# Kernel optimization log

Hardware: AMD Instinct MI355X
Metric: run time of the kernel (lower is better)

## Reference

```python
import jax, jax.numpy as jnp
import numpy as np

NEG_SLOPE = 0.2


def setup_inputs() -> dict:
    key = jax.random.key(0)
    k1, k2, k3 = jax.random.split(key, 3)
    B, C, F_in, F_out = 8, 2048, 64, 64
    node_features = jax.random.normal(k1, (B, C, F_in), dtype=jnp.float32)
    # nn.Linear weight: [out_features, in_features]
    W = jax.random.normal(k2, (F_out, F_in), dtype=jnp.float32) * (1.0 / np.sqrt(F_in))
    # attention vector a: [2*F_out, 1], xavier-uniform style init
    bound = float(np.sqrt(6.0 / (2 * F_out + 1)))
    a = jax.random.uniform(k3, (2 * F_out, 1), dtype=jnp.float32, minval=-bound, maxval=bound)
    return {"node_features": node_features, "W": W, "a": a}


def reference(node_features, W, a):
    # Wh: [B, C, F_out]
    Wh = jnp.einsum("bcf,of->bco", node_features, W)
    F_out = W.shape[0]
    a1 = a[:F_out, 0]  # scores for the i (row) side
    a2 = a[F_out:, 0]  # scores for the j (col) side
    # Decompose concat([Wh_i, Wh_j]) @ a == Wh_i@a1 + Wh_j@a2 (avoids [B,C,C,2F] tensor)
    s1 = Wh @ a1  # [B, C]
    s2 = Wh @ a2  # [B, C]
    e = jax.nn.leaky_relu(s1[:, :, None] + s2[:, None, :], negative_slope=NEG_SLOPE)  # [B,C,C]
    attention = jax.nn.softmax(e, axis=-1)
    out = jnp.einsum("bij,bjo->bio", attention, Wh)  # weighted aggregate
    return jax.nn.elu(out), attention
```

## Files before the change

kernel.cpp:

```cpp
#include <hip/hip_runtime.h>

typedef float f32x4 __attribute__((ext_vector_type(4)));
typedef _Float16 half8 __attribute__((ext_vector_type(8)));

#define NEG 0.2f

__global__ __launch_bounds__(256) void gat_wh_kernel(
    const float* __restrict__ nf, const float* __restrict__ W,
    const float* __restrict__ a, _Float16* __restrict__ whT,
    float* __restrict__ s1g, float* __restrict__ s2g, float* __restrict__ smax)
{
    const int b    = blockIdx.x >> 5;
    const int rb   = blockIdx.x & 31;
    const int row0 = rb * 64;
    const int t    = threadIdx.x;
    const int lane = t & 63;
    const int wv   = t >> 6;

    __shared__ _Float16 whL[64][72];
    __shared__ float    wred[4];

    f32x4 Wreg[16];
    const float* wp = W + lane * 64;
#pragma unroll
    for (int i = 0; i < 16; ++i) Wreg[i] = *(const f32x4*)(wp + i * 4);
    const float a1v = a[lane];
    const float a2v = a[64 + lane];

    const float* nfb = nf + ((long)b * 2048 + row0) * 64;
    float wmax = -3.0e38f;

    for (int g = 0; g < 16; ++g) {
        const int row = g * 4 + wv;
        const f32x4* nfp = (const f32x4*)(nfb + row * 64);
        f32x4 acc = {0.f, 0.f, 0.f, 0.f};
#pragma unroll
        for (int i = 0; i < 16; ++i) acc += nfp[i] * Wreg[i];
        const float wh = acc.x + acc.y + acc.z + acc.w;
        whL[row][lane] = (_Float16)wh;
        float p1 = wh * a1v;
        float p2 = wh * a2v;
#pragma unroll
        for (int m = 32; m >= 1; m >>= 1) {
            p1 += __shfl_xor(p1, m);
            p2 += __shfl_xor(p2, m);
        }
        if (lane == 0) {
            s1g[b * 2048 + row0 + row] = p1;
            s2g[b * 2048 + row0 + row] = p2;
            wmax = fmaxf(wmax, p2);
        }
    }
    if (lane == 0) wred[wv] = wmax;
    __syncthreads();
    if (t == 0)
        smax[blockIdx.x] = fmaxf(fmaxf(wred[0], wred[1]), fmaxf(wred[2], wred[3]));

    const int o = t >> 2;
    const int part = t & 3;
    unsigned int tmp[8];
#pragma unroll
    for (int kk = 0; kk < 8; ++kk) {
        const int j = part * 16 + kk * 2;
        unsigned int lo = *(const unsigned short*)&whL[j][o];
        unsigned int hi = *(const unsigned short*)&whL[j + 1][o];
        tmp[kk] = lo | (hi << 16);
    }
    uint4 v0, v1;
    v0.x = tmp[0]; v0.y = tmp[1]; v0.z = tmp[2]; v0.w = tmp[3];
    v1.x = tmp[4]; v1.y = tmp[5]; v1.z = tmp[6]; v1.w = tmp[7];
    _Float16* dst = whT + ((long)(b * 64 + o) * 2048 + row0 + part * 16);
    *(uint4*)dst = v0;
    *(uint4*)(dst + 8) = v1;
}

__global__ __launch_bounds__(256) void gat_attn_kernel(
    const _Float16* __restrict__ whT, const float* __restrict__ s1g,
    const float* __restrict__ s2g, const float* __restrict__ smax,
    float* __restrict__ outp)
{
    const int b    = blockIdx.x >> 6;
    const int rb   = blockIdx.x & 63;
    const int i0   = rb * 32;
    const int t    = threadIdx.x;
    const int lane = t & 63;
    const int wv   = t >> 6;

    __shared__ __attribute__((aligned(16))) float s2sh[2048];
    __shared__ float s1sh[32], Msh[32], iDsh[32];
    __shared__ float m2sh;
    __shared__ __attribute__((aligned(16))) _Float16 Pl[32][72];
    __shared__ __attribute__((aligned(16))) _Float16 WhL[64][72];

#pragma unroll
    for (int k = 0; k < 8; ++k) s2sh[t + k * 256] = s2g[b * 2048 + t + k * 256];
    if (t < 32) {
        s1sh[t] = s1g[b * 2048 + i0 + t];
        float v = smax[b * 32 + t];
#pragma unroll
        for (int m = 16; m >= 1; m >>= 1) v = fmaxf(v, __shfl_xor(v, m));
        if (t == 0) m2sh = v;
    }
    __syncthreads();

    {
        const float m2  = m2sh;
        const int   r   = t >> 3, q = t & 7;
        const float s1r = s1sh[r];
        const float xm  = s1r + m2;
        const float M   = fmaxf(xm, NEG * xm);
        float acc = 0.f;
        for (int j = q; j < 2048; j += 8) {
            float x = s1r + s2sh[j];
            float e = fmaxf(x, NEG * x);
            acc += __expf(e - M);
        }
        acc += __shfl_xor(acc, 1);
        acc += __shfl_xor(acc, 2);
        acc += __shfl_xor(acc, 4);
        if (q == 0) { Msh[r] = M; iDsh[r] = 1.0f / acc; }
    }
    __syncthreads();

    f32x4 acc0 = {0.f, 0.f, 0.f, 0.f}, acc1 = {0.f, 0.f, 0.f, 0.f};
    const int h  = wv & 1;
    const int cb = (wv >> 1) * 32;
    float* attnb = outp + 1048576 + ((long)b * 2048 + i0) * 2048;
    const _Float16* whTb = whT + (long)b * 64 * 2048;
    const int so = t >> 2, sp = t & 3;

    for (int c = 0; c < 32; ++c) {
        const int j0 = c * 64;
        {
            const uint4* src = (const uint4*)(whTb + (long)so * 2048 + j0 + sp * 16);
            uint4 w0 = src[0], w1 = src[1];
            *(uint4*)&WhL[so][sp * 16]     = w0;
            *(uint4*)&WhL[so][sp * 16 + 8] = w1;
        }
        const float sv = s2sh[j0 + lane];
#pragma unroll
        for (int k = 0; k < 8; ++k) {
            const int r = wv + k * 4;
            float x = s1sh[r] + sv;
            float e = fmaxf(x, NEG * x);
            float p = __expf(e - Msh[r]) * iDsh[r];
            attnb[(long)r * 2048 + j0 + lane] = p;
            Pl[r][lane] = (_Float16)p;
        }
        __syncthreads();
        {
            const int arow  = h * 16 + (lane & 15);
            const int koff  = (lane >> 4) * 8;
            const int brow0 = cb + (lane & 15);
#pragma unroll
            for (int kc = 0; kc < 2; ++kc) {
                half8 av  = *(const half8*)&Pl[arow][kc * 32 + koff];
                half8 bv0 = *(const half8*)&WhL[brow0][kc * 32 + koff];
                half8 bv1 = *(const half8*)&WhL[brow0 + 16][kc * 32 + koff];
                acc0 = __builtin_amdgcn_mfma_f32_16x16x32_f16(av, bv0, acc0, 0, 0, 0);
                acc1 = __builtin_amdgcn_mfma_f32_16x16x32_f16(av, bv1, acc1, 0, 0, 0);
            }
        }
        __syncthreads();
    }

    {
        const int col = lane & 15;
        const int rg  = lane >> 4;
        float* ob = outp + ((long)b * 2048 + i0 + h * 16 + rg * 4) * 64 + cb + col;
#pragma unroll
        for (int r = 0; r < 4; ++r) {
            float x = acc0[r];
            ob[r * 64] = (x > 0.f) ? x : (__expf(x) - 1.0f);
            float y = acc1[r];
            ob[r * 64 + 16] = (y > 0.f) ? y : (__expf(y) - 1.0f);
        }
    }
}

extern "C" void kernel_launch(void* const* d_in, const int* in_sizes, int n_in,
                              void* d_out, int out_size, void* d_ws, size_t ws_size,
                              hipStream_t stream)
{
    (void)in_sizes; (void)n_in; (void)out_size; (void)ws_size;
    const float* nf = (const float*)d_in[0];
    const float* W  = (const float*)d_in[1];
    const float* a  = (const float*)d_in[2];
    float* outp = (float*)d_out;

    char* ws = (char*)d_ws;
    _Float16* whT = (_Float16*)ws;
    float* s1g  = (float*)(ws + 2097152);
    float* s2g  = (float*)(ws + 2097152 + 65536);
    float* smax = (float*)(ws + 2097152 + 131072);

    gat_wh_kernel<<<256, 256, 0, stream>>>(nf, W, a, whT, s1g, s2g, smax);
    gat_attn_kernel<<<512, 256, 0, stream>>>(whT, s1g, s2g, smax, outp);
}
```

Before: 68.91 us.

## Compute attention probabilities directly in MFMA register layout, drop LDS staging and barriers

Result: slower. 86.60 us (+25.7%).

```diff
diff --git a/kernel.cpp b/kernel.cpp
--- a/kernel.cpp
+++ b/kernel.cpp
@@ -89,8 +89,6 @@
     __shared__ __attribute__((aligned(16))) float s2sh[2048];
     __shared__ float s1sh[32], Msh[32], iDsh[32];
     __shared__ float m2sh;
-    __shared__ __attribute__((aligned(16))) _Float16 Pl[32][72];
-    __shared__ __attribute__((aligned(16))) _Float16 WhL[64][72];
 
 #pragma unroll
     for (int k = 0; k < 8; ++k) s2sh[t + k * 256] = s2g[b * 2048 + t + k * 256];
@@ -122,58 +120,70 @@
     }
     __syncthreads();
 
+    const int h    = wv & 1;
+    const int cq   = wv >> 1;
+    const int mloc = h * 16 + (lane & 15);
+    const int g    = lane >> 4;
+    const float s1r = s1sh[mloc];
+    const float Mr  = Msh[mloc];
+    const float iDr = iDsh[mloc];
+
     f32x4 acc0 = {0.f, 0.f, 0.f, 0.f}, acc1 = {0.f, 0.f, 0.f, 0.f};
-    const int h  = wv & 1;
-    const int cb = (wv >> 1) * 32;
-    float* attnb = outp + 1048576 + ((long)b * 2048 + i0) * 2048;
-    const _Float16* whTb = whT + (long)b * 64 * 2048;
-    const int so = t >> 2, sp = t & 3;
+    const _Float16* Bb0 = whT + (long)b * 64 * 2048 + (long)(cq * 32 + (lane & 15)) * 2048 + g * 8;
+    const _Float16* Bb1 = Bb0 + 16 * 2048;
+    float* attnr = outp + 1048576 + ((long)b * 2048 + i0 + mloc) * 2048 + cq * 32 + g * 8;
+    const float* s2p = &s2sh[g * 8];
 
     for (int c = 0; c < 32; ++c) {
         const int j0 = c * 64;
-        {
-            const uint4* src = (const uint4*)(whTb + (long)so * 2048 + j0 + sp * 16);
-            uint4 w0 = src[0], w1 = src[1];
-            *(uint4*)&WhL[so][sp * 16]     = w0;
-            *(uint4*)&WhL[so][sp * 16 + 8] = w1;
-        }
-        const float sv = s2sh[j0 + lane];
-#pragma unroll
-        for (int k = 0; k < 8; ++k) {
-            const int r = wv + k * 4;
-            float x = s1sh[r] + sv;
-            float e = fmaxf(x, NEG * x);
-            float p = __expf(e - Msh[r]) * iDsh[r];
-            attnb[(long)r * 2048 + j0 + lane] = p;
-            Pl[r][lane] = (_Float16)p;
-        }
-        __syncthreads();
-        {
-            const int arow  = h * 16 + (lane & 15);
-            const int koff  = (lane >> 4) * 8;
-            const int brow0 = cb + (lane & 15);
-#pragma unroll
-            for (int kc = 0; kc < 2; ++kc) {
-                half8 av  = *(const half8*)&Pl[arow][kc * 32 + koff];
-                half8 bv0 = *(const half8*)&WhL[brow0][kc * 32 + koff];
-                half8 bv1 = *(const half8*)&WhL[brow0 + 16][kc * 32 + koff];
-                acc0 = __builtin_amdgcn_mfma_f32_16x16x32_f16(av, bv0, acc0, 0, 0, 0);
-                acc1 = __builtin_amdgcn_mfma_f32_16x16x32_f16(av, bv1, acc1, 0, 0, 0);
-            }
-        }
-        __syncthreads();
+        half8 b00 = *(const half8*)(Bb0 + j0);
+        half8 b01 = *(const half8*)(Bb1 + j0);
+        half8 b10 = *(const half8*)(Bb0 + j0 + 32);
+        half8 b11 = *(const half8*)(Bb1 + j0 + 32);
+
+        f32x4 sa0 = *(const f32x4*)(s2p + j0);
+        f32x4 sa1 = *(const f32x4*)(s2p + j0 + 4);
+        f32x4 sb0 = *(const f32x4*)(s2p + j0 + 32);
+        f32x4 sb1 = *(const f32x4*)(s2p + j0 + 36);
+        f32x4 p00, p01, p10, p11;
+        half8 a0, a1;
+#pragma unroll
+        for (int e = 0; e < 4; ++e) {
+            float x, lr, p;
+            x = s1r + sa0[e]; lr = fmaxf(x, NEG * x);
+            p = __expf(lr - Mr) * iDr; p00[e] = p; a0[e] = (_Float16)p;
+            x = s1r + sa1[e]; lr = fmaxf(x, NEG * x);
+            p = __expf(lr - Mr) * iDr; p01[e] = p; a0[e + 4] = (_Float16)p;
+            x = s1r + sb0[e]; lr = fmaxf(x, NEG * x);
+            p = __expf(lr - Mr) * iDr; p10[e] = p; a1[e] = (_Float16)p;
+            x = s1r + sb1[e]; lr = fmaxf(x, NEG * x);
+            p = __expf(lr - Mr) * iDr; p11[e] = p; a1[e + 4] = (_Float16)p;
+        }
+
+        if (cq == 0) {
+            __builtin_nontemporal_store(p00, (f32x4*)(attnr + j0));
+            __builtin_nontemporal_store(p01, (f32x4*)(attnr + j0 + 4));
+        } else {
+            __builtin_nontemporal_store(p10, (f32x4*)(attnr + j0));
+            __builtin_nontemporal_store(p11, (f32x4*)(attnr + j0 + 4));
+        }
+
+        acc0 = __builtin_amdgcn_mfma_f32_16x16x32_f16(a0, b00, acc0, 0, 0, 0);
+        acc1 = __builtin_amdgcn_mfma_f32_16x16x32_f16(a0, b01, acc1, 0, 0, 0);
+        acc0 = __builtin_amdgcn_mfma_f32_16x16x32_f16(a1, b10, acc0, 0, 0, 0);
+        acc1 = __builtin_amdgcn_mfma_f32_16x16x32_f16(a1, b11, acc1, 0, 0, 0);
     }
 
     {
-        const int col = lane & 15;
+        const int col = cq * 32 + (lane & 15);
         const int rg  = lane >> 4;
-        float* ob = outp + ((long)b * 2048 + i0 + h * 16 + rg * 4) * 64 + cb + col;
+        float* ob = outp + ((long)b * 2048 + i0 + h * 16 + rg * 4) * 64 + col;
 #pragma unroll
         for (int r = 0; r < 4; ++r) {
             float x = acc0[r];
-            ob[r * 64] = (x > 0.f) ? x : (__expf(x) - 1.0f);
+            ob[(long)r * 64] = (x > 0.f) ? x : (__expf(x) - 1.0f);
             float y = acc1[r];
-            ob[r * 64 + 16] = (y > 0.f) ? y : (__expf(y) - 1.0f);
+            ob[(long)r * 64 + 16] = (y > 0.f) ? y : (__expf(y) - 1.0f);
         }
     }
 }
```

## Halve attention row tile, load Wh B-operand directly from global, double-buffer P

Applied to the files above, without the earlier changes.

New measurement: 72.62 us. 5.4% more time.

```diff
diff --git a/kernel.cpp b/kernel.cpp
--- a/kernel.cpp
+++ b/kernel.cpp
@@ -79,23 +79,22 @@
     const float* __restrict__ s2g, const float* __restrict__ smax,
     float* __restrict__ outp)
 {
-    const int b    = blockIdx.x >> 6;
-    const int rb   = blockIdx.x & 63;
-    const int i0   = rb * 32;
+    const int b    = blockIdx.x >> 7;
+    const int rb   = blockIdx.x & 127;
+    const int i0   = rb * 16;
     const int t    = threadIdx.x;
     const int lane = t & 63;
     const int wv   = t >> 6;
 
     __shared__ __attribute__((aligned(16))) float s2sh[2048];
-    __shared__ float s1sh[32], Msh[32], iDsh[32];
+    __shared__ float s1sh[16], Msh[16], iDsh[16];
     __shared__ float m2sh;
-    __shared__ __attribute__((aligned(16))) _Float16 Pl[32][72];
-    __shared__ __attribute__((aligned(16))) _Float16 WhL[64][72];
+    __shared__ __attribute__((aligned(16))) _Float16 Pl[2][16][72];
 
 #pragma unroll
     for (int k = 0; k < 8; ++k) s2sh[t + k * 256] = s2g[b * 2048 + t + k * 256];
+    if (t < 16) s1sh[t] = s1g[b * 2048 + i0 + t];
     if (t < 32) {
-        s1sh[t] = s1g[b * 2048 + i0 + t];
         float v = smax[b * 32 + t];
 #pragma unroll
         for (int m = 16; m >= 1; m >>= 1) v = fmaxf(v, __shfl_xor(v, m));
@@ -105,12 +104,12 @@
 
     {
         const float m2  = m2sh;
-        const int   r   = t >> 3, q = t & 7;
+        const int   r   = t >> 4, q = t & 15;
         const float s1r = s1sh[r];
         const float xm  = s1r + m2;
         const float M   = fmaxf(xm, NEG * xm);
         float acc = 0.f;
-        for (int j = q; j < 2048; j += 8) {
+        for (int j = q; j < 2048; j += 16) {
             float x = s1r + s2sh[j];
             float e = fmaxf(x, NEG * x);
             acc += __expf(e - M);
@@ -118,62 +117,56 @@
         acc += __shfl_xor(acc, 1);
         acc += __shfl_xor(acc, 2);
         acc += __shfl_xor(acc, 4);
+        acc += __shfl_xor(acc, 8);
         if (q == 0) { Msh[r] = M; iDsh[r] = 1.0f / acc; }
     }
     __syncthreads();
 
-    f32x4 acc0 = {0.f, 0.f, 0.f, 0.f}, acc1 = {0.f, 0.f, 0.f, 0.f};
-    const int h  = wv & 1;
-    const int cb = (wv >> 1) * 32;
-    float* attnb = outp + 1048576 + ((long)b * 2048 + i0) * 2048;
-    const _Float16* whTb = whT + (long)b * 64 * 2048;
-    const int so = t >> 2, sp = t & 3;
+    float s1v[4], Mv[4], iDv[4];
+#pragma unroll
+    for (int k = 0; k < 4; ++k) {
+        s1v[k] = s1sh[wv * 4 + k];
+        Mv[k]  = Msh[wv * 4 + k];
+        iDv[k] = iDsh[wv * 4 + k];
+    }
+
+    f32x4 acc0 = {0.f, 0.f, 0.f, 0.f};
+    const int koff = (lane >> 4) * 8;
+    const _Float16* Bp = whT + (long)b * 64 * 2048
+                       + (long)(wv * 16 + (lane & 15)) * 2048 + koff;
+    float* attnb = outp + 1048576 + ((long)b * 2048 + i0 + wv * 4) * 2048;
 
     for (int c = 0; c < 32; ++c) {
-        const int j0 = c * 64;
-        {
-            const uint4* src = (const uint4*)(whTb + (long)so * 2048 + j0 + sp * 16);
-            uint4 w0 = src[0], w1 = src[1];
-            *(uint4*)&WhL[so][sp * 16]     = w0;
-            *(uint4*)&WhL[so][sp * 16 + 8] = w1;
-        }
+        const int j0  = c * 64;
+        const int buf = c & 1;
+
+        half8 b0 = *(const half8*)(Bp + j0);
+        half8 b1 = *(const half8*)(Bp + j0 + 32);
+
         const float sv = s2sh[j0 + lane];
 #pragma unroll
-        for (int k = 0; k < 8; ++k) {
-            const int r = wv + k * 4;
-            float x = s1sh[r] + sv;
+        for (int k = 0; k < 4; ++k) {
+            float x = s1v[k] + sv;
             float e = fmaxf(x, NEG * x);
-            float p = __expf(e - Msh[r]) * iDsh[r];
-            attnb[(long)r * 2048 + j0 + lane] = p;
-            Pl[r][lane] = (_Float16)p;
+            float p = __expf(e - Mv[k]) * iDv[k];
+            attnb[(long)k * 2048 + j0 + lane] = p;
+            Pl[buf][wv * 4 + k][lane] = (_Float16)p;
         }
         __syncthreads();
-        {
-            const int arow  = h * 16 + (lane & 15);
-            const int koff  = (lane >> 4) * 8;
-            const int brow0 = cb + (lane & 15);
-#pragma unroll
-            for (int kc = 0; kc < 2; ++kc) {
-                half8 av  = *(const half8*)&Pl[arow][kc * 32 + koff];
-                half8 bv0 = *(const half8*)&WhL[brow0][kc * 32 + koff];
-                half8 bv1 = *(const half8*)&WhL[brow0 + 16][kc * 32 + koff];
-                acc0 = __builtin_amdgcn_mfma_f32_16x16x32_f16(av, bv0, acc0, 0, 0, 0);
-                acc1 = __builtin_amdgcn_mfma_f32_16x16x32_f16(av, bv1, acc1, 0, 0, 0);
-            }
-        }
-        __syncthreads();
+
+        half8 a0 = *(const half8*)&Pl[buf][lane & 15][koff];
+        half8 a1 = *(const half8*)&Pl[buf][lane & 15][koff + 32];
+        acc0 = __builtin_amdgcn_mfma_f32_16x16x32_f16(a0, b0, acc0, 0, 0, 0);
+        acc0 = __builtin_amdgcn_mfma_f32_16x16x32_f16(a1, b1, acc0, 0, 0, 0);
     }
 
     {
-        const int col = lane & 15;
-        const int rg  = lane >> 4;
-        float* ob = outp + ((long)b * 2048 + i0 + h * 16 + rg * 4) * 64 + cb + col;
+        const int col = wv * 16 + (lane & 15);
+        float* ob = outp + ((long)b * 2048 + i0 + (lane >> 4) * 4) * 64 + col;
 #pragma unroll
         for (int r = 0; r < 4; ++r) {
             float x = acc0[r];
-            ob[r * 64] = (x > 0.f) ? x : (__expf(x) - 1.0f);
-            float y = acc1[r];
-            ob[r * 64 + 16] = (y > 0.f) ? y : (__expf(y) - 1.0f);
+            ob[(long)r * 64] = (x > 0.f) ? x : (__expf(x) - 1.0f);
         }
     }
 }
@@ -195,5 +188,5 @@
     float* smax = (float*)(ws + 2097152 + 131072);
 
     gat_wh_kernel<<<256, 256, 0, stream>>>(nf, W, a, whT, s1g, s2g, smax);
-    gat_attn_kernel<<<512, 256, 0, stream>>>(whT, s1g, s2g, smax, outp);
+    gat_attn_kernel<<<1024, 256, 0, stream>>>(whT, s1g, s2g, smax, outp);
 }
```
